# Kernel tuning notes

Measured on AMD Instinct MI355X. Metric: run time of the kernel, lower is better.

Reference implementation:

```python
import jax, jax.numpy as jnp
import numpy as np

NUM_NODES = 8192
IN_FEATURES = 1024
OUT_FEATURES = 512
NUM_EDGES = 262144  # avg degree 32


def setup_inputs() -> dict:
    key = jax.random.key(0)
    k_x, k_w, k_b, k_src, k_dst = jax.random.split(key, 5)
    x = jax.random.normal(k_x, (NUM_NODES, IN_FEATURES), dtype=jnp.float32)
    # torch nn.Linear layout: weight [out, in], bias [out]
    W = jax.random.normal(k_w, (OUT_FEATURES, IN_FEATURES), dtype=jnp.float32) * (1.0 / np.sqrt(IN_FEATURES))
    b = jax.random.normal(k_b, (OUT_FEATURES,), dtype=jnp.float32) * 0.01
    src = jax.random.randint(k_src, (NUM_EDGES,), 0, NUM_NODES, dtype=jnp.int64)
    dst = jax.random.randint(k_dst, (NUM_EDGES,), 0, NUM_NODES, dtype=jnp.int64)
    edge_index = jnp.stack([src, dst], axis=0)
    return {"x": x, "W": W, "b": b, "edge_index": edge_index, "num_nodes": NUM_NODES}


def reference(x, W, b, edge_index, num_nodes):
    # Faithful to the torch module: build dense adjacency from edge list
    # (duplicate edges collapse to 1.0 via assignment semantics),
    # linear, (dropout p=0 -> identity), dense adj @ hidden, relu.
    adj = jnp.zeros((num_nodes, num_nodes), dtype=x.dtype)
    adj = adj.at[edge_index[0], edge_index[1]].set(1.0)
    hidden = x @ W.T + b            # [N, out]
    support = adj @ hidden          # [N, out] aggregation over neighbors
    return jax.nn.relu(support)
```

## Files before the change

kernel.cpp:

```cpp
#include <hip/hip_runtime.h>

#define N_NODES 8192
#define IN_F    1024
#define OUT_F   512
#define N_EDGES 262144
#define STRIDE  96

#define HID_OFF     0u
#define XB_OFF      8388608u
#define WB_OFF      25165824u
#define DEG_OFF     26214400u
#define COL_OFF     26247168u
#define MAX_DEG     STRIDE

typedef short  bf16x8 __attribute__((ext_vector_type(8)));
typedef float  f32x4  __attribute__((ext_vector_type(4)));

__device__ __forceinline__ unsigned short f2bf(float f) {
    unsigned u = __float_as_uint(f);
    u += 0x7fffu + ((u >> 16) & 1u);
    return (unsigned short)(u >> 16);
}

__device__ __forceinline__ float bflo(unsigned u) { return __uint_as_float(u << 16); }
__device__ __forceinline__ float bfhi(unsigned u) { return __uint_as_float(u & 0xffff0000u); }

__device__ __forceinline__ void ld_lds16(const void* g, void* l) {
    __builtin_amdgcn_global_load_lds(
        (const __attribute__((address_space(1))) void*)g,
        (__attribute__((address_space(3))) void*)l, 16, 0, 0);
}

#define NX8 (N_NODES * IN_F / 8)
#define NW8 (OUT_F * IN_F / 8)
__global__ __launch_bounds__(256) void cvt_bf16_all(const float* __restrict__ x,
                                                    const float* __restrict__ w,
                                                    unsigned short* __restrict__ xb,
                                                    int* __restrict__ deg) {
    int i = blockIdx.x * blockDim.x + threadIdx.x;
    if (i < N_NODES) deg[i] = 0;
    if (i >= NX8 + NW8) return;
    const f32x4* p = (i < NX8) ? ((const f32x4*)x + (size_t)i * 2)
                               : ((const f32x4*)w + (size_t)(i - NX8) * 2);
    f32x4 v0 = __builtin_nontemporal_load(p);
    f32x4 v1 = __builtin_nontemporal_load(p + 1);
    uint4 o;
    o.x = (unsigned)f2bf(v0.x) | ((unsigned)f2bf(v0.y) << 16);
    o.y = (unsigned)f2bf(v0.z) | ((unsigned)f2bf(v0.w) << 16);
    o.z = (unsigned)f2bf(v1.x) | ((unsigned)f2bf(v1.y) << 16);
    o.w = (unsigned)f2bf(v1.z) | ((unsigned)f2bf(v1.w) << 16);
    *((uint4*)xb + i) = o;
}

#define GEMM_BLOCKS 512

__global__ __launch_bounds__(256, 2) void gemm_scatter(const unsigned short* __restrict__ Xb,
                                                       const unsigned short* __restrict__ Wb,
                                                       const float* __restrict__ bias,
                                                       unsigned short* __restrict__ H,
                                                       const int* __restrict__ src,
                                                       const int* __restrict__ dst,
                                                       int* __restrict__ deg,
                                                       int* __restrict__ col) {
    __shared__ unsigned short As[2][128 * 64];
    __shared__ unsigned short Bs[2][64 * 64];

    const int bid = blockIdx.x;
    const int tid = threadIdx.x;

    if (bid >= GEMM_BLOCKS) {
        int e = (bid - GEMM_BLOCKS) * 256 + tid;
        int s = src[e];
        int slot = atomicAdd(&deg[s], 1);
        if (slot < STRIDE) col[s * STRIDE + slot] = dst[e];
        return;
    }

    const int lane = tid & 63;
    const int wave = tid >> 6;
    const int row0 = (bid & 63) * 128;
    const int col0 = (bid >> 6) * 64;
    const int wm   = (wave & 1) * 64;
    const int wn   = (wave >> 1) * 32;
    const int fm   = lane & 15;
    const int fm7  = fm & 7;
    const int q    = lane >> 4;

    f32x4 acc[4][2];
#pragma unroll
    for (int i = 0; i < 4; ++i)
#pragma unroll
        for (int j = 0; j < 2; ++j) acc[i][j] = (f32x4)0.f;

    const int r0 = tid >> 3;
    const int kp = ((tid & 7) ^ (r0 & 7)) * 8;
    const unsigned short* Xbase = Xb + (size_t)(row0 + r0) * IN_F + kp;
    const unsigned short* Wbase = Wb + (size_t)(col0 + r0) * IN_F + kp;

#define STAGE(buf, k0) do {                                                   \
    ld_lds16(Xbase            + (k0), &As[buf][tid * 8]);                     \
    ld_lds16(Xbase + 32*IN_F  + (k0), &As[buf][(tid + 256) * 8]);             \
    ld_lds16(Xbase + 64*IN_F  + (k0), &As[buf][(tid + 512) * 8]);             \
    ld_lds16(Xbase + 96*IN_F  + (k0), &As[buf][(tid + 768) * 8]);             \
    ld_lds16(Wbase            + (k0), &Bs[buf][tid * 8]);                     \
    ld_lds16(Wbase + 32*IN_F  + (k0), &Bs[buf][(tid + 256) * 8]);             \
} while (0)

#define COMPUTE(buf) do {                                                     \
    _Pragma("unroll")                                                         \
    for (int s = 0; s < 2; ++s) {                                             \
        const int kq = s * 4 + q;                                             \
        bf16x8 a[4], b[2];                                                    \
        _Pragma("unroll")                                                     \
        for (int mi = 0; mi < 4; ++mi)                                        \
            a[mi] = *(const bf16x8*)&As[buf][(((wm + mi*16 + fm) << 3) + (kq ^ fm7)) << 3]; \
        _Pragma("unroll")                                                     \
        for (int ni = 0; ni < 2; ++ni)                                        \
            b[ni] = *(const bf16x8*)&Bs[buf][(((wn + ni*16 + fm) << 3) + (kq ^ fm7)) << 3]; \
        _Pragma("unroll")                                                     \
        for (int mi = 0; mi < 4; ++mi)                                        \
            _Pragma("unroll")                                                 \
            for (int ni = 0; ni < 2; ++ni)                                    \
                acc[mi][ni] = __builtin_amdgcn_mfma_f32_16x16x32_bf16(        \
                    a[mi], b[ni], acc[mi][ni], 0, 0, 0);                      \
    }                                                                         \
} while (0)

    STAGE(0, 0);
    __syncthreads();
    int cur = 0;
    for (int t = 0; t < 15; ++t) {
        STAGE(cur ^ 1, (t + 1) * 64);
        COMPUTE(cur);
        __syncthreads();
        cur ^= 1;
    }
    COMPUTE(cur);

    const int cm = (lane >> 4) * 4;
#pragma unroll
    for (int ni = 0; ni < 2; ++ni) {
        const int c = col0 + wn + ni * 16 + fm;
        const float bv = bias[c];
#pragma unroll
        for (int mi = 0; mi < 4; ++mi) {
#pragma unroll
            for (int r = 0; r < 4; ++r) {
                const int row = row0 + wm + mi * 16 + cm + r;
                H[(size_t)row * OUT_F + c] = f2bf(acc[mi][ni][r] + bv);
            }
        }
    }
#undef STAGE
#undef COMPUTE
}

__global__ __launch_bounds__(256) void aggregate(const unsigned short* __restrict__ H,
                                                 const int* __restrict__ dg,
                                                 const int* __restrict__ col,
                                                 float* __restrict__ out) {
    __shared__ int nbr[4][MAX_DEG];
    __shared__ int uniq[4][MAX_DEG];
    __shared__ int wcnt[4];
    const int wave = threadIdx.x >> 6;
    const int lane = threadIdx.x & 63;
    const int v    = blockIdx.x * 4 + wave;
    int d = dg[v];
    if (d > MAX_DEG) d = MAX_DEG;

    if (lane == 0) wcnt[wave] = 0;
    int id0 = -1, id1 = -1;
    if (lane < d)      { id0 = col[v * STRIDE + lane];      nbr[wave][lane]      = id0; }
    if (64 + lane < d) { id1 = col[v * STRIDE + 64 + lane]; nbr[wave][64 + lane] = id1; }
    __builtin_amdgcn_wave_barrier();

    bool k0 = (lane < d);
    const int lim0 = k0 ? lane : 0;
    for (int j = 0; j < lim0; ++j) k0 = k0 & (nbr[wave][j] != id0);
    bool k1 = (64 + lane < d);
    const int lim1 = k1 ? (64 + lane) : 0;
    for (int j = 0; j < lim1; ++j) k1 = k1 & (nbr[wave][j] != id1);
    if (k0) uniq[wave][atomicAdd(&wcnt[wave], 1)] = id0;
    if (k1) uniq[wave][atomicAdd(&wcnt[wave], 1)] = id1;
    __builtin_amdgcn_wave_barrier();
    const int n  = wcnt[wave];
    const int f0 = lane * 8;

    float a0=0,a1=0,a2=0,a3=0,a4=0,a5=0,a6=0,a7=0;
    int e = 0;
    for (; e + 8 <= n; e += 8) {
        const int i0 = uniq[wave][e],   i1 = uniq[wave][e+1],
                  i2 = uniq[wave][e+2], i3 = uniq[wave][e+3],
                  i4 = uniq[wave][e+4], i5 = uniq[wave][e+5],
                  i6 = uniq[wave][e+6], i7 = uniq[wave][e+7];
        uint4 h0 = *(const uint4*)&H[(size_t)i0 * OUT_F + f0];
        uint4 h1 = *(const uint4*)&H[(size_t)i1 * OUT_F + f0];
        uint4 h2 = *(const uint4*)&H[(size_t)i2 * OUT_F + f0];
        uint4 h3 = *(const uint4*)&H[(size_t)i3 * OUT_F + f0];
        uint4 h4 = *(const uint4*)&H[(size_t)i4 * OUT_F + f0];
        uint4 h5 = *(const uint4*)&H[(size_t)i5 * OUT_F + f0];
        uint4 h6 = *(const uint4*)&H[(size_t)i6 * OUT_F + f0];
        uint4 h7 = *(const uint4*)&H[(size_t)i7 * OUT_F + f0];
        a0 += (bflo(h0.x)+bflo(h1.x)) + (bflo(h2.x)+bflo(h3.x))
            + (bflo(h4.x)+bflo(h5.x)) + (bflo(h6.x)+bflo(h7.x));
        a1 += (bfhi(h0.x)+bfhi(h1.x)) + (bfhi(h2.x)+bfhi(h3.x))
            + (bfhi(h4.x)+bfhi(h5.x)) + (bfhi(h6.x)+bfhi(h7.x));
        a2 += (bflo(h0.y)+bflo(h1.y)) + (bflo(h2.y)+bflo(h3.y))
            + (bflo(h4.y)+bflo(h5.y)) + (bflo(h6.y)+bflo(h7.y));
        a3 += (bfhi(h0.y)+bfhi(h1.y)) + (bfhi(h2.y)+bfhi(h3.y))
            + (bfhi(h4.y)+bfhi(h5.y)) + (bfhi(h6.y)+bfhi(h7.y));
        a4 += (bflo(h0.z)+bflo(h1.z)) + (bflo(h2.z)+bflo(h3.z))
            + (bflo(h4.z)+bflo(h5.z)) + (bflo(h6.z)+bflo(h7.z));
        a5 += (bfhi(h0.z)+bfhi(h1.z)) + (bfhi(h2.z)+bfhi(h3.z))
            + (bfhi(h4.z)+bfhi(h5.z)) + (bfhi(h6.z)+bfhi(h7.z));
        a6 += (bflo(h0.w)+bflo(h1.w)) + (bflo(h2.w)+bflo(h3.w))
            + (bflo(h4.w)+bflo(h5.w)) + (bflo(h6.w)+bflo(h7.w));
        a7 += (bfhi(h0.w)+bfhi(h1.w)) + (bfhi(h2.w)+bfhi(h3.w))
            + (bfhi(h4.w)+bfhi(h5.w)) + (bfhi(h6.w)+bfhi(h7.w));
    }
    for (; e + 4 <= n; e += 4) {
        const int i0 = uniq[wave][e], i1 = uniq[wave][e+1],
                  i2 = uniq[wave][e+2], i3 = uniq[wave][e+3];
        uint4 h0 = *(const uint4*)&H[(size_t)i0 * OUT_F + f0];
        uint4 h1 = *(const uint4*)&H[(size_t)i1 * OUT_F + f0];
        uint4 h2 = *(const uint4*)&H[(size_t)i2 * OUT_F + f0];
        uint4 h3 = *(const uint4*)&H[(size_t)i3 * OUT_F + f0];
        a0 += bflo(h0.x)+bflo(h1.x)+bflo(h2.x)+bflo(h3.x);
        a1 += bfhi(h0.x)+bfhi(h1.x)+bfhi(h2.x)+bfhi(h3.x);
        a2 += bflo(h0.y)+bflo(h1.y)+bflo(h2.y)+bflo(h3.y);
        a3 += bfhi(h0.y)+bfhi(h1.y)+bfhi(h2.y)+bfhi(h3.y);
        a4 += bflo(h0.z)+bflo(h1.z)+bflo(h2.z)+bflo(h3.z);
        a5 += bfhi(h0.z)+bfhi(h1.z)+bfhi(h2.z)+bfhi(h3.z);
        a6 += bflo(h0.w)+bflo(h1.w)+bflo(h2.w)+bflo(h3.w);
        a7 += bfhi(h0.w)+bfhi(h1.w)+bfhi(h2.w)+bfhi(h3.w);
    }
    for (; e < n; ++e) {
        uint4 h0 = *(const uint4*)&H[(size_t)uniq[wave][e] * OUT_F + f0];
        a0 += bflo(h0.x); a1 += bfhi(h0.x);
        a2 += bflo(h0.y); a3 += bfhi(h0.y);
        a4 += bflo(h0.z); a5 += bfhi(h0.z);
        a6 += bflo(h0.w); a7 += bfhi(h0.w);
    }
    f32x4 o0 = {fmaxf(a0,0.f), fmaxf(a1,0.f), fmaxf(a2,0.f), fmaxf(a3,0.f)};
    f32x4 o1 = {fmaxf(a4,0.f), fmaxf(a5,0.f), fmaxf(a6,0.f), fmaxf(a7,0.f)};
    __builtin_nontemporal_store(o0, (f32x4*)&out[(size_t)v * OUT_F + f0]);
    __builtin_nontemporal_store(o1, (f32x4*)&out[(size_t)v * OUT_F + f0 + 4]);
}

extern "C" void kernel_launch(void* const* d_in, const int* in_sizes, int n_in,
                              void* d_out, int out_size, void* d_ws, size_t ws_size,
                              hipStream_t stream) {
    const float* x  = (const float*)d_in[0];
    const float* W  = (const float*)d_in[1];
    const float* b  = (const float*)d_in[2];
    const int*   ei = (const int*)d_in[3];
    float* out = (float*)d_out;

    char* ws = (char*)d_ws;
    unsigned short* H   = (unsigned short*)(ws + HID_OFF);
    unsigned short* Xb  = (unsigned short*)(ws + XB_OFF);
    unsigned short* Wb  = (unsigned short*)(ws + WB_OFF);
    int*            deg = (int*)(ws + DEG_OFF);
    int*            col = (int*)(ws + COL_OFF);

    cvt_bf16_all<<<(NX8 + NW8 + 255) / 256, 256, 0, stream>>>(x, W, Xb, deg);

    gemm_scatter<<<GEMM_BLOCKS + N_EDGES / 256, 256, 0, stream>>>(Xb, Wb, b, H, ei, ei + N_EDGES, deg, col);

    aggregate<<<N_NODES / 4, 256, 0, stream>>>(H, deg, col, out);
}
```

Baseline: 139.6 us.

## Move edge scatter into conversion kernel and deepen aggregate gather unroll

The edge-list scatter (degree atomics and column fill) moves out of the GEMM launch and into the bf16 conversion kernel, with the degree array cleared by a separate memset beforehand. The GEMM kernel now runs only its 512 tiles, so its tail no longer waits on scatter blocks. The aggregate kernel gathers 16 neighbor rows per iteration instead of 8 to keep more loads in flight, and gets a launch-bounds occupancy hint. The cost is an extra memset launch and higher register pressure in the aggregate loop.

```diff
diff --git a/kernel.cpp b/kernel.cpp
--- a/kernel.cpp
+++ b/kernel.cpp
@@ -33,12 +33,23 @@
 
 #define NX8 (N_NODES * IN_F / 8)
 #define NW8 (OUT_F * IN_F / 8)
-__global__ __launch_bounds__(256) void cvt_bf16_all(const float* __restrict__ x,
-                                                    const float* __restrict__ w,
-                                                    unsigned short* __restrict__ xb,
-                                                    int* __restrict__ deg) {
-    int i = blockIdx.x * blockDim.x + threadIdx.x;
-    if (i < N_NODES) deg[i] = 0;
+#define SCAT_BLOCKS 1024
+__global__ __launch_bounds__(256) void cvt_scatter(const float* __restrict__ x,
+                                                   const float* __restrict__ w,
+                                                   unsigned short* __restrict__ xb,
+                                                   const int* __restrict__ src,
+                                                   const int* __restrict__ dst,
+                                                   int* __restrict__ deg,
+                                                   int* __restrict__ col) {
+    const int bid = blockIdx.x;
+    if (bid < SCAT_BLOCKS) {
+        int e = bid * 256 + threadIdx.x;
+        int s = src[e];
+        int slot = atomicAdd(&deg[s], 1);
+        if (slot < STRIDE) col[s * STRIDE + slot] = dst[e];
+        return;
+    }
+    int i = (bid - SCAT_BLOCKS) * 256 + threadIdx.x;
     if (i >= NX8 + NW8) return;
     const f32x4* p = (i < NX8) ? ((const f32x4*)x + (size_t)i * 2)
                                : ((const f32x4*)w + (size_t)(i - NX8) * 2);
@@ -52,30 +63,15 @@
     *((uint4*)xb + i) = o;
 }
 
-#define GEMM_BLOCKS 512
-
-__global__ __launch_bounds__(256, 2) void gemm_scatter(const unsigned short* __restrict__ Xb,
-                                                       const unsigned short* __restrict__ Wb,
-                                                       const float* __restrict__ bias,
-                                                       unsigned short* __restrict__ H,
-                                                       const int* __restrict__ src,
-                                                       const int* __restrict__ dst,
-                                                       int* __restrict__ deg,
-                                                       int* __restrict__ col) {
+__global__ __launch_bounds__(256, 2) void gemm(const unsigned short* __restrict__ Xb,
+                                               const unsigned short* __restrict__ Wb,
+                                               const float* __restrict__ bias,
+                                               unsigned short* __restrict__ H) {
     __shared__ unsigned short As[2][128 * 64];
     __shared__ unsigned short Bs[2][64 * 64];
 
     const int bid = blockIdx.x;
     const int tid = threadIdx.x;
-
-    if (bid >= GEMM_BLOCKS) {
-        int e = (bid - GEMM_BLOCKS) * 256 + tid;
-        int s = src[e];
-        int slot = atomicAdd(&deg[s], 1);
-        if (slot < STRIDE) col[s * STRIDE + slot] = dst[e];
-        return;
-    }
-
     const int lane = tid & 63;
     const int wave = tid >> 6;
     const int row0 = (bid & 63) * 128;
@@ -155,10 +151,10 @@
 #undef COMPUTE
 }
 
-__global__ __launch_bounds__(256) void aggregate(const unsigned short* __restrict__ H,
-                                                 const int* __restrict__ dg,
-                                                 const int* __restrict__ col,
-                                                 float* __restrict__ out) {
+__global__ __launch_bounds__(256, 4) void aggregate(const unsigned short* __restrict__ H,
+                                                    const int* __restrict__ dg,
+                                                    const int* __restrict__ col,
+                                                    float* __restrict__ out) {
     __shared__ int nbr[4][MAX_DEG];
     __shared__ int uniq[4][MAX_DEG];
     __shared__ int wcnt[4];
@@ -185,57 +181,38 @@
     __builtin_amdgcn_wave_barrier();
     const int n  = wcnt[wave];
     const int f0 = lane * 8;
+    const int* uq = &uniq[wave][0];
 
     float a0=0,a1=0,a2=0,a3=0,a4=0,a5=0,a6=0,a7=0;
     int e = 0;
-    for (; e + 8 <= n; e += 8) {
-        const int i0 = uniq[wave][e],   i1 = uniq[wave][e+1],
-                  i2 = uniq[wave][e+2], i3 = uniq[wave][e+3],
-                  i4 = uniq[wave][e+4], i5 = uniq[wave][e+5],
-                  i6 = uniq[wave][e+6], i7 = uniq[wave][e+7];
-        uint4 h0 = *(const uint4*)&H[(size_t)i0 * OUT_F + f0];
-        uint4 h1 = *(const uint4*)&H[(size_t)i1 * OUT_F + f0];
-        uint4 h2 = *(const uint4*)&H[(size_t)i2 * OUT_F + f0];
-        uint4 h3 = *(const uint4*)&H[(size_t)i3 * OUT_F + f0];
-        uint4 h4 = *(const uint4*)&H[(size_t)i4 * OUT_F + f0];
-        uint4 h5 = *(const uint4*)&H[(size_t)i5 * OUT_F + f0];
-        uint4 h6 = *(const uint4*)&H[(size_t)i6 * OUT_F + f0];
-        uint4 h7 = *(const uint4*)&H[(size_t)i7 * OUT_F + f0];
-        a0 += (bflo(h0.x)+bflo(h1.x)) + (bflo(h2.x)+bflo(h3.x))
-            + (bflo(h4.x)+bflo(h5.x)) + (bflo(h6.x)+bflo(h7.x));
-        a1 += (bfhi(h0.x)+bfhi(h1.x)) + (bfhi(h2.x)+bfhi(h3.x))
-            + (bfhi(h4.x)+bfhi(h5.x)) + (bfhi(h6.x)+bfhi(h7.x));
-        a2 += (bflo(h0.y)+bflo(h1.y)) + (bflo(h2.y)+bflo(h3.y))
-            + (bflo(h4.y)+bflo(h5.y)) + (bflo(h6.y)+bflo(h7.y));
-        a3 += (bfhi(h0.y)+bfhi(h1.y)) + (bfhi(h2.y)+bfhi(h3.y))
-            + (bfhi(h4.y)+bfhi(h5.y)) + (bfhi(h6.y)+bfhi(h7.y));
-        a4 += (bflo(h0.z)+bflo(h1.z)) + (bflo(h2.z)+bflo(h3.z))
-            + (bflo(h4.z)+bflo(h5.z)) + (bflo(h6.z)+bflo(h7.z));
-        a5 += (bfhi(h0.z)+bfhi(h1.z)) + (bfhi(h2.z)+bfhi(h3.z))
-            + (bfhi(h4.z)+bfhi(h5.z)) + (bfhi(h6.z)+bfhi(h7.z));
-        a6 += (bflo(h0.w)+bflo(h1.w)) + (bflo(h2.w)+bflo(h3.w))
-            + (bflo(h4.w)+bflo(h5.w)) + (bflo(h6.w)+bflo(h7.w));
-        a7 += (bfhi(h0.w)+bfhi(h1.w)) + (bfhi(h2.w)+bfhi(h3.w))
-            + (bfhi(h4.w)+bfhi(h5.w)) + (bfhi(h6.w)+bfhi(h7.w));
+    for (; e + 16 <= n; e += 16) {
+        uint4 h[16];
+#pragma unroll
+        for (int t = 0; t < 16; ++t)
+            h[t] = *(const uint4*)&H[(size_t)uq[e + t] * OUT_F + f0];
+#pragma unroll
+        for (int t = 0; t < 16; ++t) {
+            a0 += bflo(h[t].x); a1 += bfhi(h[t].x);
+            a2 += bflo(h[t].y); a3 += bfhi(h[t].y);
+            a4 += bflo(h[t].z); a5 += bfhi(h[t].z);
+            a6 += bflo(h[t].w); a7 += bfhi(h[t].w);
+        }
     }
     for (; e + 4 <= n; e += 4) {
-        const int i0 = uniq[wave][e], i1 = uniq[wave][e+1],
-                  i2 = uniq[wave][e+2], i3 = uniq[wave][e+3];
-        uint4 h0 = *(const uint4*)&H[(size_t)i0 * OUT_F + f0];
-        uint4 h1 = *(const uint4*)&H[(size_t)i1 * OUT_F + f0];
-        uint4 h2 = *(const uint4*)&H[(size_t)i2 * OUT_F + f0];
-        uint4 h3 = *(const uint4*)&H[(size_t)i3 * OUT_F + f0];
-        a0 += bflo(h0.x)+bflo(h1.x)+bflo(h2.x)+bflo(h3.x);
-        a1 += bfhi(h0.x)+bfhi(h1.x)+bfhi(h2.x)+bfhi(h3.x);
-        a2 += bflo(h0.y)+bflo(h1.y)+bflo(h2.y)+bflo(h3.y);
-        a3 += bfhi(h0.y)+bfhi(h1.y)+bfhi(h2.y)+bfhi(h3.y);
-        a4 += bflo(h0.z)+bflo(h1.z)+bflo(h2.z)+bflo(h3.z);
-        a5 += bfhi(h0.z)+bfhi(h1.z)+bfhi(h2.z)+bfhi(h3.z);
-        a6 += bflo(h0.w)+bflo(h1.w)+bflo(h2.w)+bflo(h3.w);
-        a7 += bfhi(h0.w)+bfhi(h1.w)+bfhi(h2.w)+bfhi(h3.w);
+        uint4 h[4];
+#pragma unroll
+        for (int t = 0; t < 4; ++t)
+            h[t] = *(const uint4*)&H[(size_t)uq[e + t] * OUT_F + f0];
+#pragma unroll
+        for (int t = 0; t < 4; ++t) {
+            a0 += bflo(h[t].x); a1 += bfhi(h[t].x);
+            a2 += bflo(h[t].y); a3 += bfhi(h[t].y);
+            a4 += bflo(h[t].z); a5 += bfhi(h[t].z);
+            a6 += bflo(h[t].w); a7 += bfhi(h[t].w);
+        }
     }
     for (; e < n; ++e) {
-        uint4 h0 = *(const uint4*)&H[(size_t)uniq[wave][e] * OUT_F + f0];
+        uint4 h0 = *(const uint4*)&H[(size_t)uq[e] * OUT_F + f0];
         a0 += bflo(h0.x); a1 += bfhi(h0.x);
         a2 += bflo(h0.y); a3 += bfhi(h0.y);
         a4 += bflo(h0.z); a5 += bfhi(h0.z);
@@ -263,9 +240,12 @@
     int*            deg = (int*)(ws + DEG_OFF);
     int*            col = (int*)(ws + COL_OFF);
 
-    cvt_bf16_all<<<(NX8 + NW8 + 255) / 256, 256, 0, stream>>>(x, W, Xb, deg);
-
-    gemm_scatter<<<GEMM_BLOCKS + N_EDGES / 256, 256, 0, stream>>>(Xb, Wb, b, H, ei, ei + N_EDGES, deg, col);
+    hipMemsetAsync(deg, 0, N_NODES * sizeof(int), stream);
+
+    cvt_scatter<<<SCAT_BLOCKS + (NX8 + NW8) / 256, 256, 0, stream>>>(
+        x, W, Xb, ei, ei + N_EDGES, deg, col);
+
+    gemm<<<512, 256, 0, stream>>>(Xb, Wb, b, H);
 
     aggregate<<<N_NODES / 4, 256, 0, stream>>>(H, deg, col, out);
 }
```

New measurement: 147.8 us. 1.06x slower.
